# Optimization experiments

Hardware: AMD Instinct MI355X
Metric: run time of the kernel (lower is better)

The kernel has to match this reference:

```python
import jax, jax.numpy as jnp
import numpy as np

B, NQ, NK, D = 8, 4096, 4096, 512


def setup_inputs() -> dict:
    key = jax.random.key(0)
    ks = jax.random.split(key, 8)
    s = 1.0 / np.sqrt(D)
    return {
        "x": jax.random.normal(ks[0], (B, NQ, D), dtype=jnp.float32),
        "context": jax.random.normal(ks[1], (B, NK, D), dtype=jnp.float32),
        "Wq": jax.random.normal(ks[2], (D, D), dtype=jnp.float32) * s,
        "bq": jax.random.normal(ks[3], (D,), dtype=jnp.float32) * 0.01,
        "Wk": jax.random.normal(ks[4], (D, D), dtype=jnp.float32) * s,
        "bk": jax.random.normal(ks[5], (D,), dtype=jnp.float32) * 0.01,
        "Wv": jax.random.normal(ks[6], (D, D), dtype=jnp.float32) * s,
        "bv": jax.random.normal(ks[7], (D,), dtype=jnp.float32) * 0.01,
    }


def reference(x, context, Wq, bq, Wk, bk, Wv, bv):
    # torch Linear: y = x @ W.T + b, W is [out, in]
    Q = jnp.einsum('bnd,ed->bne', x, Wq) + bq          # [B, NQ, D]
    K = jnp.einsum('bmd,ed->bme', context, Wk) + bk    # [B, NK, D]
    V = jnp.einsum('bmd,ed->bme', context, Wv) + bv    # [B, NK, D]
    scale = 1.0 / jnp.sqrt(jnp.asarray(x.shape[-1], dtype=x.dtype))
    scores = jnp.einsum('bne,bme->bnm', Q, K) * scale  # [B, NQ, NK]
    attn = jax.nn.softmax(scores, axis=-1)
    return jnp.einsum('bnm,bme->bne', attn, V)         # [B, NQ, D]
```

## Files before the change

### kernel.cpp

```cpp
#include <hip/hip_runtime.h>
#include <math.h>

typedef unsigned short u16;
typedef unsigned int u32;
typedef __attribute__((ext_vector_type(8))) short short8;
typedef __attribute__((ext_vector_type(4))) float floatx4;

#define DEVINL static __device__ __forceinline__

DEVINL u16 f2b(float f) {
  u32 u = __float_as_uint(f);
  u += 0x7FFFu + ((u >> 16) & 1u);
  return (u16)(u >> 16);
}

DEVINL void gload16(const void* g, void* lds_base) {
  __builtin_amdgcn_global_load_lds(
      (const __attribute__((address_space(1))) void*)g,
      (__attribute__((address_space(3))) void*)lds_base, 16, 0, 0);
}

DEVINL void stage_a_f32(const float* __restrict__ A, int lda, int gm0, int k0,
                        u16* As, int tid) {
  const int idx = tid & 127;
  const int row8 = idx >> 4;
  const int k16h = idx & 15;
  const int chsel = tid >> 7;
#pragma unroll
  for (int rr = 0; rr < 8; ++rr) {
    const int chunk = rr * 2 + chsel;
    const float4 v = *(const float4*)(A + (long)(gm0 + chunk * 8 + row8) * lda + k0 + k16h * 4);
    u32 lo = (u32)f2b(v.x) | ((u32)f2b(v.y) << 16);
    u32 hi = (u32)f2b(v.z) | ((u32)f2b(v.w) << 16);
    const int baddr = chunk * 1024 + row8 * 128 + (((k16h >> 1) ^ row8) << 4) + ((k16h & 1) << 3);
    uint2 p; p.x = lo; p.y = hi;
    *(uint2*)((char*)As + baddr) = p;
  }
}

__global__ __launch_bounds__(256) void cast4_kernel(const float* __restrict__ in,
                                                    u16* __restrict__ out, long n4) {
  long i = (long)blockIdx.x * blockDim.x + threadIdx.x;
  long stride = (long)gridDim.x * blockDim.x;
  for (; i < n4; i += stride) {
    float4 v = ((const float4*)in)[i];
    ushort4 o;
    o.x = f2b(v.x); o.y = f2b(v.y); o.z = f2b(v.z); o.w = f2b(v.w);
    ((ushort4*)out)[i] = o;
  }
}

__global__ __launch_bounds__(256) void zerof(float* __restrict__ p, int n4) {
  int i = blockIdx.x * 256 + threadIdx.x;
  if (i < n4) ((float4*)p)[i] = make_float4(0.f, 0.f, 0.f, 0.f);
}

__global__ __launch_bounds__(256) void proj_q(const float* __restrict__ A,
                                              const u16* __restrict__ Bt,
                                              const float* __restrict__ bias,
                                              u16* __restrict__ C) {
  __shared__ u16 As[8192];
  __shared__ u16 Bs[8192];
  const int tid = threadIdx.x;
  const int lane = tid & 63;
  const int wave = tid >> 6;
  const int gm0 = blockIdx.y * 128;
  const int gn0 = blockIdx.x * 128;
  const int wm = (wave >> 1) * 64;
  const int wn = (wave & 1) * 64;

  floatx4 acc[4][4];
#pragma unroll
  for (int i = 0; i < 4; ++i)
#pragma unroll
    for (int j = 0; j < 4; ++j)
#pragma unroll
      for (int r = 0; r < 4; ++r) acc[i][j][r] = 0.0f;

  const int lrow = lane >> 3;
  const int lcol = (lane & 7) ^ lrow;
  const int fr_row = lane & 15;
  const int fr_k16 = lane >> 4;

  for (int k0 = 0; k0 < 512; k0 += 64) {
#pragma unroll
    for (int c = 0; c < 4; ++c) {
      const int ch = wave * 4 + c;
      gload16(Bt + (long)(gn0 + ch * 8 + lrow) * 512 + k0 + lcol * 8, (char*)Bs + ch * 1024);
    }
    stage_a_f32(A, 512, gm0, k0, As, tid);
    __syncthreads();
#pragma unroll
    for (int ks = 0; ks < 2; ++ks) {
      const int c16 = ks * 4 + fr_k16;
      short8 af[4], bfv[4];
#pragma unroll
      for (int i = 0; i < 4; ++i) {
        const int m = wm + i * 16 + fr_row;
        const int slot = (m >> 3) * 64 + (m & 7) * 8 + (c16 ^ (m & 7));
        af[i] = *(const short8*)((const char*)As + slot * 16);
      }
#pragma unroll
      for (int j = 0; j < 4; ++j) {
        const int n = wn + j * 16 + fr_row;
        const int slot = (n >> 3) * 64 + (n & 7) * 8 + (c16 ^ (n & 7));
        bfv[j] = *(const short8*)((const char*)Bs + slot * 16);
      }
#pragma unroll
      for (int i = 0; i < 4; ++i)
#pragma unroll
        for (int j = 0; j < 4; ++j)
          acc[i][j] = __builtin_amdgcn_mfma_f32_16x16x32_bf16(af[i], bfv[j], acc[i][j], 0, 0, 0);
    }
    __syncthreads();
  }

  const int crow = (lane >> 4) * 4;
  const int ccol = lane & 15;
#pragma unroll
  for (int i = 0; i < 4; ++i)
#pragma unroll
    for (int j = 0; j < 4; ++j) {
      const int n = gn0 + wn + j * 16 + ccol;
      const float badd = bias[n];
#pragma unroll
      for (int r = 0; r < 4; ++r) {
        const int m = gm0 + wm + i * 16 + crow + r;
        C[(long)m * 512 + n] = f2b(acc[i][j][r] + badd);
      }
    }
}

__global__ __launch_bounds__(256) void proj_kv(const float* __restrict__ A,
                                               const u16* __restrict__ Wk,
                                               const float* __restrict__ bk,
                                               const u16* __restrict__ Wv,
                                               const float* __restrict__ bv,
                                               u16* __restrict__ Kb,
                                               u16* __restrict__ Vt) {
  __shared__ u16 As[8192];
  __shared__ u16 Bs[8192];
  const int tid = threadIdx.x;
  const int lane = tid & 63;
  const int wave = tid >> 6;
  const int isV = blockIdx.x >> 2;
  const u16* Bt = isV ? Wv : Wk;
  const float* bias = isV ? bv : bk;
  const int gm0 = blockIdx.y * 128;
  const int gn0 = (blockIdx.x & 3) * 128;
  const int wm = (wave >> 1) * 64;
  const int wn = (wave & 1) * 64;

  floatx4 acc[4][4];
#pragma unroll
  for (int i = 0; i < 4; ++i)
#pragma unroll
    for (int j = 0; j < 4; ++j)
#pragma unroll
      for (int r = 0; r < 4; ++r) acc[i][j][r] = 0.0f;

  const int lrow = lane >> 3;
  const int lcol = (lane & 7) ^ lrow;
  const int fr_row = lane & 15;
  const int fr_k16 = lane >> 4;

  for (int k0 = 0; k0 < 512; k0 += 64) {
#pragma unroll
    for (int c = 0; c < 4; ++c) {
      const int ch = wave * 4 + c;
      gload16(Bt + (long)(gn0 + ch * 8 + lrow) * 512 + k0 + lcol * 8, (char*)Bs + ch * 1024);
    }
    stage_a_f32(A, 512, gm0, k0, As, tid);
    __syncthreads();
#pragma unroll
    for (int ks = 0; ks < 2; ++ks) {
      const int c16 = ks * 4 + fr_k16;
      short8 af[4], bfv[4];
#pragma unroll
      for (int i = 0; i < 4; ++i) {
        const int m = wm + i * 16 + fr_row;
        const int slot = (m >> 3) * 64 + (m & 7) * 8 + (c16 ^ (m & 7));
        af[i] = *(const short8*)((const char*)As + slot * 16);
      }
#pragma unroll
      for (int j = 0; j < 4; ++j) {
        const int n = wn + j * 16 + fr_row;
        const int slot = (n >> 3) * 64 + (n & 7) * 8 + (c16 ^ (n & 7));
        bfv[j] = *(const short8*)((const char*)Bs + slot * 16);
      }
#pragma unroll
      for (int i = 0; i < 4; ++i)
#pragma unroll
        for (int j = 0; j < 4; ++j)
          acc[i][j] = __builtin_amdgcn_mfma_f32_16x16x32_bf16(af[i], bfv[j], acc[i][j], 0, 0, 0);
    }
    __syncthreads();
  }

  const int crow = (lane >> 4) * 4;
  const int ccol = lane & 15;
  if (!isV) {
#pragma unroll
    for (int i = 0; i < 4; ++i)
#pragma unroll
      for (int j = 0; j < 4; ++j) {
        const int n = gn0 + wn + j * 16 + ccol;
        const float badd = bias[n];
#pragma unroll
        for (int r = 0; r < 4; ++r) {
          const int m = gm0 + wm + i * 16 + crow + r;
          Kb[(long)m * 512 + n] = f2b(acc[i][j][r] + badd);
        }
      }
  } else {
#pragma unroll
    for (int i = 0; i < 4; ++i)
#pragma unroll
      for (int j = 0; j < 4; ++j) {
        const int n = gn0 + wn + j * 16 + ccol;
        const float badd = bias[j < 0 ? 0 : n];
        const int m = gm0 + wm + i * 16 + crow;
        const int b = m >> 12;
        const int mm = m & 4095;
        ushort4 st;
        st.x = f2b(acc[i][j][0] + badd);
        st.y = f2b(acc[i][j][1] + badd);
        st.z = f2b(acc[i][j][2] + badd);
        st.w = f2b(acc[i][j][3] + badd);
        *(ushort4*)(Vt + (long)b * 512 * 4096 + (long)n * 4096 + mm) = st;
      }
  }
}

__global__ __launch_bounds__(256) void gemm_s(
    const u16* __restrict__ A, const u16* __restrict__ Bt, u16* __restrict__ S,
    float* __restrict__ Ld, float scale, long aBS, long bBS) {
  __shared__ u16 As[8192];
  __shared__ u16 Bs[8192];
  const int tid = threadIdx.x;
  const int lane = tid & 63;
  const int wave = tid >> 6;
  const int bz = blockIdx.z;
  A += (long)bz * aBS;
  Bt += (long)bz * bBS;
  u16* Sb = S + (long)bz * 4096 * 4096;
  const int gm0 = blockIdx.y * 128;
  const int gn0 = blockIdx.x * 128;
  const int wm = (wave >> 1) * 64;
  const int wn = (wave & 1) * 64;

  floatx4 acc[4][4];
#pragma unroll
  for (int i = 0; i < 4; ++i)
#pragma unroll
    for (int j = 0; j < 4; ++j)
#pragma unroll
      for (int r = 0; r < 4; ++r) acc[i][j][r] = 0.0f;

  const int lrow = lane >> 3;
  const int lcol = (lane & 7) ^ lrow;
  const int fr_row = lane & 15;
  const int fr_k16 = lane >> 4;

  for (int k0 = 0; k0 < 512; k0 += 64) {
#pragma unroll
    for (int c = 0; c < 4; ++c) {
      const int ch = wave * 4 + c;
      const int r = ch * 8 + lrow;
      gload16(A + (long)(gm0 + r) * 512 + k0 + lcol * 8, (char*)As + ch * 1024);
      gload16(Bt + (long)(gn0 + r) * 512 + k0 + lcol * 8, (char*)Bs + ch * 1024);
    }
    __syncthreads();
#pragma unroll
    for (int ks = 0; ks < 2; ++ks) {
      const int c16 = ks * 4 + fr_k16;
      short8 af[4], bfv[4];
#pragma unroll
      for (int i = 0; i < 4; ++i) {
        const int m = wm + i * 16 + fr_row;
        const int slot = (m >> 3) * 64 + (m & 7) * 8 + (c16 ^ (m & 7));
        af[i] = *(const short8*)((const char*)As + slot * 16);
      }
#pragma unroll
      for (int j = 0; j < 4; ++j) {
        const int n = wn + j * 16 + fr_row;
        const int slot = (n >> 3) * 64 + (n & 7) * 8 + (c16 ^ (n & 7));
        bfv[j] = *(const short8*)((const char*)Bs + slot * 16);
      }
#pragma unroll
      for (int i = 0; i < 4; ++i)
#pragma unroll
        for (int j = 0; j < 4; ++j)
          acc[i][j] = __builtin_amdgcn_mfma_f32_16x16x32_bf16(af[i], bfv[j], acc[i][j], 0, 0, 0);
    }
    __syncthreads();
  }

  const int crow = (lane >> 4) * 4;
  const int ccol = lane & 15;
  float (*sml)[2] = (float (*)[2])As;
#pragma unroll
  for (int i = 0; i < 4; ++i) {
#pragma unroll
    for (int r = 0; r < 4; ++r) {
      const int m = gm0 + wm + i * 16 + crow + r;
      float p = 0.0f;
#pragma unroll
      for (int j = 0; j < 4; ++j) {
        const int n = gn0 + wn + j * 16 + ccol;
        const float e = __expf(acc[i][j][r] * scale);
        Sb[(long)m * 4096 + n] = f2b(e);
        p += e;
      }
#pragma unroll
      for (int off = 1; off < 16; off <<= 1) p += __shfl_xor(p, off, 64);
      if ((lane & 15) == 0) sml[wm + i * 16 + crow + r][wave & 1] = p;
    }
  }
  __syncthreads();
  if (tid < 128)
    atomicAdd(&Ld[(long)bz * 4096 + gm0 + tid], sml[tid][0] + sml[tid][1]);
}

__global__ __launch_bounds__(256) void gemm_o(
    const u16* __restrict__ A, const u16* __restrict__ Bt, float* __restrict__ Cout,
    const float* __restrict__ Ld, long aBS, long bBS, long cBS) {
  __shared__ u16 As[8192];
  __shared__ u16 Bs[8192];
  const int tid = threadIdx.x;
  const int lane = tid & 63;
  const int wave = tid >> 6;
  const int bz = blockIdx.z;
  A += (long)bz * aBS;
  Bt += (long)bz * bBS;
  const long cbase = (long)bz * cBS;
  const int gm0 = blockIdx.y * 128;
  const int gn0 = blockIdx.x * 128;
  const int wm = (wave >> 1) * 64;
  const int wn = (wave & 1) * 64;

  floatx4 acc[4][4];
#pragma unroll
  for (int i = 0; i < 4; ++i)
#pragma unroll
    for (int j = 0; j < 4; ++j)
#pragma unroll
      for (int r = 0; r < 4; ++r) acc[i][j][r] = 0.0f;

  const int lrow = lane >> 3;
  const int lcol = (lane & 7) ^ lrow;
  const int fr_row = lane & 15;
  const int fr_k16 = lane >> 4;

  for (int k0 = 0; k0 < 4096; k0 += 64) {
#pragma unroll
    for (int c = 0; c < 4; ++c) {
      const int ch = wave * 4 + c;
      const int r = ch * 8 + lrow;
      gload16(A + (long)(gm0 + r) * 4096 + k0 + lcol * 8, (char*)As + ch * 1024);
      gload16(Bt + (long)(gn0 + r) * 4096 + k0 + lcol * 8, (char*)Bs + ch * 1024);
    }
    __syncthreads();
#pragma unroll
    for (int ks = 0; ks < 2; ++ks) {
      const int c16 = ks * 4 + fr_k16;
      short8 af[4], bfv[4];
#pragma unroll
      for (int i = 0; i < 4; ++i) {
        const int m = wm + i * 16 + fr_row;
        const int slot = (m >> 3) * 64 + (m & 7) * 8 + (c16 ^ (m & 7));
        af[i] = *(const short8*)((const char*)As + slot * 16);
      }
#pragma unroll
      for (int j = 0; j < 4; ++j) {
        const int n = wn + j * 16 + fr_row;
        const int slot = (n >> 3) * 64 + (n & 7) * 8 + (c16 ^ (n & 7));
        bfv[j] = *(const short8*)((const char*)Bs + slot * 16);
      }
#pragma unroll
      for (int i = 0; i < 4; ++i)
#pragma unroll
        for (int j = 0; j < 4; ++j)
          acc[i][j] = __builtin_amdgcn_mfma_f32_16x16x32_bf16(af[i], bfv[j], acc[i][j], 0, 0, 0);
    }
    __syncthreads();
  }

  const int crow = (lane >> 4) * 4;
  const int ccol = lane & 15;
  float linv[4][4];
#pragma unroll
  for (int i = 0; i < 4; ++i)
#pragma unroll
    for (int r = 0; r < 4; ++r)
      linv[i][r] = 1.0f / Ld[(long)bz * 4096 + gm0 + wm + i * 16 + crow + r];
#pragma unroll
  for (int i = 0; i < 4; ++i)
#pragma unroll
    for (int j = 0; j < 4; ++j) {
      const int n = gn0 + wn + j * 16 + ccol;
#pragma unroll
      for (int r = 0; r < 4; ++r) {
        const int m = gm0 + wm + i * 16 + crow + r;
        Cout[cbase + (long)m * 512 + n] = acc[i][j][r] * linv[i][r];
      }
    }
}

extern "C" void kernel_launch(void* const* d_in, const int* in_sizes, int n_in,
                              void* d_out, int out_size, void* d_ws, size_t ws_size,
                              hipStream_t stream) {
  const int B = 8, NQ = 4096, NK = 4096, D = 512;
  const long nX = (long)B * NQ * D;
  const long nW = (long)D * D;
  const float scale = 0.044194173824159216f;

  const float* x = (const float*)d_in[0];
  const float* ctx = (const float*)d_in[1];
  const float* Wq = (const float*)d_in[2];
  const float* bq = (const float*)d_in[3];
  const float* Wk = (const float*)d_in[4];
  const float* bk = (const float*)d_in[5];
  const float* Wv = (const float*)d_in[6];
  const float* bv = (const float*)d_in[7];
  float* out = (float*)d_out;

  size_t off = 0;
  auto alloc = [&](size_t bytes) { size_t o = off; off = (off + bytes + 255) & ~(size_t)255; return o; };
  char* ws = (char*)d_ws;
  u16* Qb  = (u16*)(ws + alloc(nX * 2));
  u16* Kb  = (u16*)(ws + alloc(nX * 2));
  u16* Vt  = (u16*)(ws + alloc(nX * 2));
  float* Ld = (float*)(ws + alloc((size_t)B * NQ * 4));
  const size_t s_off = off;
  u16* wqb = (u16*)(ws + alloc(nW * 2));
  u16* wkb = (u16*)(ws + alloc(nW * 2));
  u16* wvb = (u16*)(ws + alloc(nW * 2));
  u16* S   = (u16*)(ws + s_off);

  const size_t sBatch = (size_t)NQ * NK * 2;
  const size_t avail = (ws_size > s_off) ? (ws_size - s_off) : 0;
  int nb = (int)(avail / sBatch);
  if (nb > 8) nb = 8;
  else if (nb >= 4 && nb < 8) nb = 4;
  if (nb < 1) nb = 1;

  cast4_kernel<<<128, 256, 0, stream>>>(Wq, wqb, nW / 4);
  cast4_kernel<<<128, 256, 0, stream>>>(Wk, wkb, nW / 4);
  cast4_kernel<<<128, 256, 0, stream>>>(Wv, wvb, nW / 4);
  zerof<<<(B * NQ / 4 + 255) / 256, 256, 0, stream>>>(Ld, B * NQ / 4);

  proj_q<<<dim3(4, 256), 256, 0, stream>>>(x, wqb, bq, Qb);
  proj_kv<<<dim3(8, 256), 256, 0, stream>>>(ctx, wkb, bk, wvb, bv, Kb, Vt);

  for (int b0 = 0; b0 < B; b0 += nb) {
    const int nbb = (b0 + nb <= B) ? nb : (B - b0);
    gemm_s<<<dim3(32, 32, nbb), 256, 0, stream>>>(
        Qb + (long)b0 * NQ * D, Kb + (long)b0 * NK * D, S,
        Ld + (long)b0 * NQ, scale, (long)NQ * D, (long)NK * D);
    gemm_o<<<dim3(4, 32, nbb), 256, 0, stream>>>(
        S, Vt + (long)b0 * D * NK, out + (long)b0 * NQ * D,
        Ld + (long)b0 * NQ, (long)NQ * NK, (long)D * NK, (long)NQ * D);
  }
  (void)in_sizes; (void)n_in; (void)out_size;
}
```

Before: 776.3 us.

## Fold softmax scale into Q, use hardware bf16 pack and exp2, retile PV GEMM

```diff
diff --git a/kernel.cpp b/kernel.cpp
--- a/kernel.cpp
+++ b/kernel.cpp
@@ -8,10 +8,15 @@
 
 #define DEVINL static __device__ __forceinline__
 
-DEVINL u16 f2b(float f) {
-  u32 u = __float_as_uint(f);
-  u += 0x7FFFu + ((u >> 16) & 1u);
-  return (u16)(u >> 16);
+DEVINL u32 pk2(float a, float b) {
+  u32 r;
+  asm("v_cvt_pk_bf16_f32 %0, %1, %2" : "=v"(r) : "v"(a), "v"(b));
+  return r;
+}
+DEVINL float exp2fast(float x) {
+  float r;
+  asm("v_exp_f32 %0, %1" : "=v"(r) : "v"(x));
+  return r;
 }
 
 DEVINL void gload16(const void* g, void* lds_base) {
@@ -30,10 +35,8 @@
   for (int rr = 0; rr < 8; ++rr) {
     const int chunk = rr * 2 + chsel;
     const float4 v = *(const float4*)(A + (long)(gm0 + chunk * 8 + row8) * lda + k0 + k16h * 4);
-    u32 lo = (u32)f2b(v.x) | ((u32)f2b(v.y) << 16);
-    u32 hi = (u32)f2b(v.z) | ((u32)f2b(v.w) << 16);
     const int baddr = chunk * 1024 + row8 * 128 + (((k16h >> 1) ^ row8) << 4) + ((k16h & 1) << 3);
-    uint2 p; p.x = lo; p.y = hi;
+    uint2 p; p.x = pk2(v.x, v.y); p.y = pk2(v.z, v.w);
     *(uint2*)((char*)As + baddr) = p;
   }
 }
@@ -44,9 +47,8 @@
   long stride = (long)gridDim.x * blockDim.x;
   for (; i < n4; i += stride) {
     float4 v = ((const float4*)in)[i];
-    ushort4 o;
-    o.x = f2b(v.x); o.y = f2b(v.y); o.z = f2b(v.z); o.w = f2b(v.w);
-    ((ushort4*)out)[i] = o;
+    uint2 o; o.x = pk2(v.x, v.y); o.y = pk2(v.z, v.w);
+    ((uint2*)out)[i] = o;
   }
 }
 
@@ -58,7 +60,7 @@
 __global__ __launch_bounds__(256) void proj_q(const float* __restrict__ A,
                                               const u16* __restrict__ Bt,
                                               const float* __restrict__ bias,
-                                              u16* __restrict__ C) {
+                                              u16* __restrict__ C, float oscale) {
   __shared__ u16 As[8192];
   __shared__ u16 Bs[8192];
   const int tid = threadIdx.x;
@@ -123,11 +125,17 @@
     for (int j = 0; j < 4; ++j) {
       const int n = gn0 + wn + j * 16 + ccol;
       const float badd = bias[n];
-#pragma unroll
-      for (int r = 0; r < 4; ++r) {
-        const int m = gm0 + wm + i * 16 + crow + r;
-        C[(long)m * 512 + n] = f2b(acc[i][j][r] + badd);
-      }
+      const float a0 = (acc[i][j][0] + badd) * oscale;
+      const float a1 = (acc[i][j][1] + badd) * oscale;
+      const float a2 = (acc[i][j][2] + badd) * oscale;
+      const float a3 = (acc[i][j][3] + badd) * oscale;
+      const u32 p01 = pk2(a0, a1);
+      const u32 p23 = pk2(a2, a3);
+      u16* cp = C + (long)(gm0 + wm + i * 16 + crow) * 512 + n;
+      cp[0]    = (u16)p01;
+      cp[512]  = (u16)(p01 >> 16);
+      cp[1024] = (u16)p23;
+      cp[1536] = (u16)(p23 >> 16);
     }
 }
 
@@ -206,11 +214,13 @@
       for (int j = 0; j < 4; ++j) {
         const int n = gn0 + wn + j * 16 + ccol;
         const float badd = bias[n];
-#pragma unroll
-        for (int r = 0; r < 4; ++r) {
-          const int m = gm0 + wm + i * 16 + crow + r;
-          Kb[(long)m * 512 + n] = f2b(acc[i][j][r] + badd);
-        }
+        const u32 p01 = pk2(acc[i][j][0] + badd, acc[i][j][1] + badd);
+        const u32 p23 = pk2(acc[i][j][2] + badd, acc[i][j][3] + badd);
+        u16* cp = Kb + (long)(gm0 + wm + i * 16 + crow) * 512 + n;
+        cp[0]    = (u16)p01;
+        cp[512]  = (u16)(p01 >> 16);
+        cp[1024] = (u16)p23;
+        cp[1536] = (u16)(p23 >> 16);
       }
   } else {
 #pragma unroll
@@ -218,23 +228,21 @@
 #pragma unroll
       for (int j = 0; j < 4; ++j) {
         const int n = gn0 + wn + j * 16 + ccol;
-        const float badd = bias[j < 0 ? 0 : n];
+        const float badd = bias[n];
         const int m = gm0 + wm + i * 16 + crow;
         const int b = m >> 12;
         const int mm = m & 4095;
-        ushort4 st;
-        st.x = f2b(acc[i][j][0] + badd);
-        st.y = f2b(acc[i][j][1] + badd);
-        st.z = f2b(acc[i][j][2] + badd);
-        st.w = f2b(acc[i][j][3] + badd);
-        *(ushort4*)(Vt + (long)b * 512 * 4096 + (long)n * 4096 + mm) = st;
+        uint2 st;
+        st.x = pk2(acc[i][j][0] + badd, acc[i][j][1] + badd);
+        st.y = pk2(acc[i][j][2] + badd, acc[i][j][3] + badd);
+        *(uint2*)(Vt + (long)b * 512 * 4096 + (long)n * 4096 + mm) = st;
       }
   }
 }
 
 __global__ __launch_bounds__(256) void gemm_s(
     const u16* __restrict__ A, const u16* __restrict__ Bt, u16* __restrict__ S,
-    float* __restrict__ Ld, float scale, long aBS, long bBS) {
+    float* __restrict__ Ld, long aBS, long bBS) {
   __shared__ u16 As[8192];
   __shared__ u16 Bs[8192];
   const int tid = threadIdx.x;
@@ -301,20 +309,36 @@
   float (*sml)[2] = (float (*)[2])As;
 #pragma unroll
   for (int i = 0; i < 4; ++i) {
-#pragma unroll
-    for (int r = 0; r < 4; ++r) {
-      const int m = gm0 + wm + i * 16 + crow + r;
-      float p = 0.0f;
-#pragma unroll
-      for (int j = 0; j < 4; ++j) {
-        const int n = gn0 + wn + j * 16 + ccol;
-        const float e = __expf(acc[i][j][r] * scale);
-        Sb[(long)m * 4096 + n] = f2b(e);
-        p += e;
-      }
-#pragma unroll
-      for (int off = 1; off < 16; off <<= 1) p += __shfl_xor(p, off, 64);
-      if ((lane & 15) == 0) sml[wm + i * 16 + crow + r][wave & 1] = p;
+    float rs0 = 0.f, rs1 = 0.f, rs2 = 0.f, rs3 = 0.f;
+    u16* sp = Sb + (long)(gm0 + wm + i * 16 + crow) * 4096 + gn0 + wn + ccol;
+#pragma unroll
+    for (int j = 0; j < 4; ++j) {
+      const float e0 = exp2fast(acc[i][j][0]);
+      const float e1 = exp2fast(acc[i][j][1]);
+      const float e2 = exp2fast(acc[i][j][2]);
+      const float e3 = exp2fast(acc[i][j][3]);
+      const u32 p01 = pk2(e0, e1);
+      const u32 p23 = pk2(e2, e3);
+      u16* q = sp + j * 16;
+      q[0]     = (u16)p01;
+      q[4096]  = (u16)(p01 >> 16);
+      q[8192]  = (u16)p23;
+      q[12288] = (u16)(p23 >> 16);
+      rs0 += e0; rs1 += e1; rs2 += e2; rs3 += e3;
+    }
+#pragma unroll
+    for (int off = 1; off < 16; off <<= 1) {
+      rs0 += __shfl_xor(rs0, off, 64);
+      rs1 += __shfl_xor(rs1, off, 64);
+      rs2 += __shfl_xor(rs2, off, 64);
+      rs3 += __shfl_xor(rs3, off, 64);
+    }
+    if ((lane & 15) == 0) {
+      const int rb = wm + i * 16 + crow;
+      sml[rb + 0][wave & 1] = rs0;
+      sml[rb + 1][wave & 1] = rs1;
+      sml[rb + 2][wave & 1] = rs2;
+      sml[rb + 3][wave & 1] = rs3;
     }
   }
   __syncthreads();
@@ -325,7 +349,7 @@
 __global__ __launch_bounds__(256) void gemm_o(
     const u16* __restrict__ A, const u16* __restrict__ Bt, float* __restrict__ Cout,
     const float* __restrict__ Ld, long aBS, long bBS, long cBS) {
-  __shared__ u16 As[8192];
+  __shared__ u16 As[4096];
   __shared__ u16 Bs[8192];
   const int tid = threadIdx.x;
   const int lane = tid & 63;
@@ -334,16 +358,15 @@
   A += (long)bz * aBS;
   Bt += (long)bz * bBS;
   const long cbase = (long)bz * cBS;
-  const int gm0 = blockIdx.y * 128;
+  const int gm0 = blockIdx.y * 64;
   const int gn0 = blockIdx.x * 128;
-  const int wm = (wave >> 1) * 64;
-  const int wn = (wave & 1) * 64;
-
-  floatx4 acc[4][4];
-#pragma unroll
-  for (int i = 0; i < 4; ++i)
-#pragma unroll
-    for (int j = 0; j < 4; ++j)
+  const int wn = wave * 32;
+
+  floatx4 acc[4][2];
+#pragma unroll
+  for (int i = 0; i < 4; ++i)
+#pragma unroll
+    for (int j = 0; j < 2; ++j)
 #pragma unroll
       for (int r = 0; r < 4; ++r) acc[i][j][r] = 0.0f;
 
@@ -354,25 +377,28 @@
 
   for (int k0 = 0; k0 < 4096; k0 += 64) {
 #pragma unroll
+    for (int c = 0; c < 2; ++c) {
+      const int ch = wave * 2 + c;
+      gload16(A + (long)(gm0 + ch * 8 + lrow) * 4096 + k0 + lcol * 8, (char*)As + ch * 1024);
+    }
+#pragma unroll
     for (int c = 0; c < 4; ++c) {
       const int ch = wave * 4 + c;
-      const int r = ch * 8 + lrow;
-      gload16(A + (long)(gm0 + r) * 4096 + k0 + lcol * 8, (char*)As + ch * 1024);
-      gload16(Bt + (long)(gn0 + r) * 4096 + k0 + lcol * 8, (char*)Bs + ch * 1024);
+      gload16(Bt + (long)(gn0 + ch * 8 + lrow) * 4096 + k0 + lcol * 8, (char*)Bs + ch * 1024);
     }
     __syncthreads();
 #pragma unroll
     for (int ks = 0; ks < 2; ++ks) {
       const int c16 = ks * 4 + fr_k16;
-      short8 af[4], bfv[4];
+      short8 af[4], bfv[2];
 #pragma unroll
       for (int i = 0; i < 4; ++i) {
-        const int m = wm + i * 16 + fr_row;
+        const int m = i * 16 + fr_row;
         const int slot = (m >> 3) * 64 + (m & 7) * 8 + (c16 ^ (m & 7));
         af[i] = *(const short8*)((const char*)As + slot * 16);
       }
 #pragma unroll
-      for (int j = 0; j < 4; ++j) {
+      for (int j = 0; j < 2; ++j) {
         const int n = wn + j * 16 + fr_row;
         const int slot = (n >> 3) * 64 + (n & 7) * 8 + (c16 ^ (n & 7));
         bfv[j] = *(const short8*)((const char*)Bs + slot * 16);
@@ -380,7 +406,7 @@
 #pragma unroll
       for (int i = 0; i < 4; ++i)
 #pragma unroll
-        for (int j = 0; j < 4; ++j)
+        for (int j = 0; j < 2; ++j)
           acc[i][j] = __builtin_amdgcn_mfma_f32_16x16x32_bf16(af[i], bfv[j], acc[i][j], 0, 0, 0);
     }
     __syncthreads();
@@ -393,15 +419,15 @@
   for (int i = 0; i < 4; ++i)
 #pragma unroll
     for (int r = 0; r < 4; ++r)
-      linv[i][r] = 1.0f / Ld[(long)bz * 4096 + gm0 + wm + i * 16 + crow + r];
-#pragma unroll
-  for (int i = 0; i < 4; ++i)
-#pragma unroll
-    for (int j = 0; j < 4; ++j) {
+      linv[i][r] = 1.0f / Ld[(long)bz * 4096 + gm0 + i * 16 + crow + r];
+#pragma unroll
+  for (int i = 0; i < 4; ++i)
+#pragma unroll
+    for (int j = 0; j < 2; ++j) {
       const int n = gn0 + wn + j * 16 + ccol;
 #pragma unroll
       for (int r = 0; r < 4; ++r) {
-        const int m = gm0 + wm + i * 16 + crow + r;
+        const int m = gm0 + i * 16 + crow + r;
         Cout[cbase + (long)m * 512 + n] = acc[i][j][r] * linv[i][r];
       }
     }
@@ -413,7 +439,7 @@
   const int B = 8, NQ = 4096, NK = 4096, D = 512;
   const long nX = (long)B * NQ * D;
   const long nW = (long)D * D;
-  const float scale = 0.044194173824159216f;
+  const float oscale = 0.044194173824159216f * 1.4426950408889634f;
 
   const float* x = (const float*)d_in[0];
   const float* ctx = (const float*)d_in[1];
@@ -450,15 +476,15 @@
   cast4_kernel<<<128, 256, 0, stream>>>(Wv, wvb, nW / 4);
   zerof<<<(B * NQ / 4 + 255) / 256, 256, 0, stream>>>(Ld, B * NQ / 4);
 
-  proj_q<<<dim3(4, 256), 256, 0, stream>>>(x, wqb, bq, Qb);
+  proj_q<<<dim3(4, 256), 256, 0, stream>>>(x, wqb, bq, Qb, oscale);
   proj_kv<<<dim3(8, 256), 256, 0, stream>>>(ctx, wkb, bk, wvb, bv, Kb, Vt);
 
   for (int b0 = 0; b0 < B; b0 += nb) {
     const int nbb = (b0 + nb <= B) ? nb : (B - b0);
     gemm_s<<<dim3(32, 32, nbb), 256, 0, stream>>>(
         Qb + (long)b0 * NQ * D, Kb + (long)b0 * NK * D, S,
-        Ld + (long)b0 * NQ, scale, (long)NQ * D, (long)NK * D);
-    gemm_o<<<dim3(4, 32, nbb), 256, 0, stream>>>(
+        Ld + (long)b0 * NQ, (long)NQ * D, (long)NK * D);
+    gemm_o<<<dim3(4, 64, nbb), 256, 0, stream>>>(
         S, Vt + (long)b0 * D * NK, out + (long)b0 * NQ * D,
         Ld + (long)b0 * NQ, (long)NQ * NK, (long)D * NK, (long)NQ * D);
   }
```

Result: faster. 745.8 us (-3.9%).
